# Kernel tuning notes

Hardware: AMD Instinct MI355X
Metric: run time of the kernel (lower is better)

Reference implementation:

```python
import jax, jax.numpy as jnp
import numpy as np

T, J, D = 65536, 512, 128

def setup_inputs() -> dict:
    key = jax.random.key(0)
    k1, k2 = jax.random.split(key)
    u = jax.random.normal(k1, (1, J, D), dtype=jnp.float32)
    s = jax.random.normal(k2, (T, J), dtype=jnp.float32)
    return {"u": u, "s": s}

def reference(u, s):
    # softmax over the query axis (axis=1 of s, matching tf softmax(s, axis=1))
    A = jax.nn.softmax(s, axis=1)          # [T, J]
    # sum_j A[t, j] * u[0, j, :]  == A @ u[0]
    c2q = jnp.einsum('tj,jd->td', A, u[0])  # [T, D]
    return c2q.T                            # [D, T], matching tf.transpose(c2q)
```

## Files before the change

kernel.cpp:

```cpp
#include <hip/hip_runtime.h>
#include <hip/hip_bf16.h>


constexpr int T_DIM = 65536;
constexpr int J_DIM = 512;
constexpr int D_DIM = 128;
constexpr int KK_STEPS = J_DIM / 32;
constexpr int NFRAG = 8;
constexpr int PF_DEPTH = 4;
constexpr int BP_ELEMS = KK_STEPS * NFRAG * 64;

typedef __attribute__((ext_vector_type(4))) float  f32x4;
typedef __attribute__((ext_vector_type(8))) short  s16x8;
typedef __attribute__((ext_vector_type(8))) __bf16 bf16x8;

__device__ __forceinline__ short f2bf_rne(float f) {
    unsigned u = __builtin_bit_cast(unsigned, f);
    u += 0x7fffu + ((u >> 16) & 1u);
    return (short)(u >> 16);
}

__global__ __launch_bounds__(256) void prep_b(const float* __restrict__ u,
                                              short* __restrict__ bp) {
    int tid = blockIdx.x * blockDim.x + threadIdx.x;
    if (tid >= BP_ELEMS) return;
    int l  = tid & 63;
    int nf = (tid >> 6) & (NFRAG - 1);
    int kk = tid >> 9;
    int d  = nf * 16 + (l & 15);
    int k0 = kk * 32 + 8 * (l >> 4);
    s16x8 o;
#pragma unroll
    for (int i = 0; i < 8; ++i)
        o[i] = f2bf_rne(u[(size_t)(k0 + i) * D_DIM + d]);
    *reinterpret_cast<s16x8*>(bp + (size_t)tid * 8) = o;
}

__global__ __launch_bounds__(512, 2) void c2q_main(const float* __restrict__ sm,
                                                   const short* __restrict__ bp,
                                                   float* __restrict__ out) {
    __shared__ s16x8 bsh[BP_ELEMS];

    const int tid  = threadIdx.x;
    const int l    = tid & 63;
    const int w    = tid >> 6;
    const int lmod = l & 15;
    const int lh   = l >> 4;
    const int r0   = blockIdx.x * 128 + w * 16;

    const float* sp = sm + (size_t)(r0 + lmod) * J_DIM + lh * 8;

    f32x4 sbuf[PF_DEPTH][2];
#pragma unroll
    for (int p = 0; p < PF_DEPTH; ++p) {
        sbuf[p][0] = *reinterpret_cast<const f32x4*>(sp + p * 32);
        sbuf[p][1] = *reinterpret_cast<const f32x4*>(sp + p * 32 + 4);
    }

    {
        const s16x8* bps = reinterpret_cast<const s16x8*>(bp);
#pragma unroll
        for (int it = 0; it < BP_ELEMS / 512; ++it)
            bsh[it * 512 + tid] = bps[it * 512 + tid];
    }
    __syncthreads();

    f32x4 acc[NFRAG];
#pragma unroll
    for (int nf = 0; nf < NFRAG; ++nf) acc[nf] = (f32x4){0.f, 0.f, 0.f, 0.f};
    float den = 0.f;

#pragma unroll
    for (int kk = 0; kk < KK_STEPS; ++kk) {
        f32x4 s0 = sbuf[kk & (PF_DEPTH - 1)][0];
        f32x4 s1 = sbuf[kk & (PF_DEPTH - 1)][1];
        if (kk + PF_DEPTH < KK_STEPS) {
            sbuf[kk & (PF_DEPTH - 1)][0] =
                *reinterpret_cast<const f32x4*>(sp + (kk + PF_DEPTH) * 32);
            sbuf[kk & (PF_DEPTH - 1)][1] =
                *reinterpret_cast<const f32x4*>(sp + (kk + PF_DEPTH) * 32 + 4);
        }
        float e0 = __expf(s0[0]), e1 = __expf(s0[1]);
        float e2 = __expf(s0[2]), e3 = __expf(s0[3]);
        float e4 = __expf(s1[0]), e5 = __expf(s1[1]);
        float e6 = __expf(s1[2]), e7 = __expf(s1[3]);
        den += ((e0 + e1) + (e2 + e3)) + ((e4 + e5) + (e6 + e7));
        s16x8 a;
        a[0] = f2bf_rne(e0); a[1] = f2bf_rne(e1);
        a[2] = f2bf_rne(e2); a[3] = f2bf_rne(e3);
        a[4] = f2bf_rne(e4); a[5] = f2bf_rne(e5);
        a[6] = f2bf_rne(e6); a[7] = f2bf_rne(e7);
        bf16x8 av = __builtin_bit_cast(bf16x8, a);
#pragma unroll
        for (int nf = 0; nf < NFRAG; ++nf) {
            bf16x8 bv = __builtin_bit_cast(bf16x8, bsh[(kk * NFRAG + nf) * 64 + l]);
            acc[nf] = __builtin_amdgcn_mfma_f32_16x16x32_bf16(av, bv, acc[nf], 0, 0, 0);
        }
        __builtin_amdgcn_sched_barrier(0);
    }

    den += __shfl_xor(den, 16, 64);
    den += __shfl_xor(den, 32, 64);
    float inv[4];
#pragma unroll
    for (int r = 0; r < 4; ++r)
        inv[r] = 1.0f / __shfl(den, 4 * lh + r, 64);

#pragma unroll
    for (int nf = 0; nf < NFRAG; ++nf) {
        f32x4 v;
#pragma unroll
        for (int r = 0; r < 4; ++r) v[r] = acc[nf][r] * inv[r];
        *reinterpret_cast<f32x4*>(out + (size_t)(nf * 16 + lmod) * T_DIM
                                  + r0 + 4 * lh) = v;
    }
}

extern "C" void kernel_launch(void* const* d_in, const int* in_sizes, int n_in,
                              void* d_out, int out_size, void* d_ws, size_t ws_size,
                              hipStream_t stream) {
    const float* u = (const float*)d_in[0];
    const float* s = (const float*)d_in[1];
    float* out = (float*)d_out;
    short* bp = (short*)d_ws;

    prep_b<<<(BP_ELEMS + 255) / 256, 256, 0, stream>>>(u, bp);
    c2q_main<<<T_DIM / 128, 512, 0, stream>>>(s, bp, out);
}
```

Baseline: 40.56 us.

## Process two row tiles per wave to reuse shared B fragments

```diff
diff --git a/kernel.cpp b/kernel.cpp
--- a/kernel.cpp
+++ b/kernel.cpp
@@ -46,15 +46,19 @@
     const int w    = tid >> 6;
     const int lmod = l & 15;
     const int lh   = l >> 4;
-    const int r0   = blockIdx.x * 128 + w * 16;
+    const int r0a  = blockIdx.x * 256 + w * 16;
+    const int r0b  = r0a + 128;
 
-    const float* sp = sm + (size_t)(r0 + lmod) * J_DIM + lh * 8;
+    const float* spA = sm + (size_t)(r0a + lmod) * J_DIM + lh * 8;
+    const float* spB = sm + (size_t)(r0b + lmod) * J_DIM + lh * 8;
 
-    f32x4 sbuf[PF_DEPTH][2];
+    f32x4 sbufA[PF_DEPTH][2], sbufB[PF_DEPTH][2];
 #pragma unroll
     for (int p = 0; p < PF_DEPTH; ++p) {
-        sbuf[p][0] = *reinterpret_cast<const f32x4*>(sp + p * 32);
-        sbuf[p][1] = *reinterpret_cast<const f32x4*>(sp + p * 32 + 4);
+        sbufA[p][0] = *reinterpret_cast<const f32x4*>(spA + p * 32);
+        sbufA[p][1] = *reinterpret_cast<const f32x4*>(spA + p * 32 + 4);
+        sbufB[p][0] = *reinterpret_cast<const f32x4*>(spB + p * 32);
+        sbufB[p][1] = *reinterpret_cast<const f32x4*>(spB + p * 32 + 4);
     }
 
     {
@@ -65,54 +69,83 @@
     }
     __syncthreads();
 
-    f32x4 acc[NFRAG];
+    f32x4 accA[NFRAG], accB[NFRAG];
 #pragma unroll
-    for (int nf = 0; nf < NFRAG; ++nf) acc[nf] = (f32x4){0.f, 0.f, 0.f, 0.f};
-    float den = 0.f;
+    for (int nf = 0; nf < NFRAG; ++nf) {
+        accA[nf] = (f32x4){0.f, 0.f, 0.f, 0.f};
+        accB[nf] = (f32x4){0.f, 0.f, 0.f, 0.f};
+    }
+    float denA = 0.f, denB = 0.f;
 
 #pragma unroll
     for (int kk = 0; kk < KK_STEPS; ++kk) {
-        f32x4 s0 = sbuf[kk & (PF_DEPTH - 1)][0];
-        f32x4 s1 = sbuf[kk & (PF_DEPTH - 1)][1];
+        f32x4 a0 = sbufA[kk & (PF_DEPTH - 1)][0];
+        f32x4 a1 = sbufA[kk & (PF_DEPTH - 1)][1];
+        f32x4 b0 = sbufB[kk & (PF_DEPTH - 1)][0];
+        f32x4 b1 = sbufB[kk & (PF_DEPTH - 1)][1];
         if (kk + PF_DEPTH < KK_STEPS) {
-            sbuf[kk & (PF_DEPTH - 1)][0] =
-                *reinterpret_cast<const f32x4*>(sp + (kk + PF_DEPTH) * 32);
-            sbuf[kk & (PF_DEPTH - 1)][1] =
-                *reinterpret_cast<const f32x4*>(sp + (kk + PF_DEPTH) * 32 + 4);
+            sbufA[kk & (PF_DEPTH - 1)][0] =
+                *reinterpret_cast<const f32x4*>(spA + (kk + PF_DEPTH) * 32);
+            sbufA[kk & (PF_DEPTH - 1)][1] =
+                *reinterpret_cast<const f32x4*>(spA + (kk + PF_DEPTH) * 32 + 4);
+            sbufB[kk & (PF_DEPTH - 1)][0] =
+                *reinterpret_cast<const f32x4*>(spB + (kk + PF_DEPTH) * 32);
+            sbufB[kk & (PF_DEPTH - 1)][1] =
+                *reinterpret_cast<const f32x4*>(spB + (kk + PF_DEPTH) * 32 + 4);
         }
-        float e0 = __expf(s0[0]), e1 = __expf(s0[1]);
-        float e2 = __expf(s0[2]), e3 = __expf(s0[3]);
-        float e4 = __expf(s1[0]), e5 = __expf(s1[1]);
-        float e6 = __expf(s1[2]), e7 = __expf(s1[3]);
-        den += ((e0 + e1) + (e2 + e3)) + ((e4 + e5) + (e6 + e7));
-        s16x8 a;
-        a[0] = f2bf_rne(e0); a[1] = f2bf_rne(e1);
-        a[2] = f2bf_rne(e2); a[3] = f2bf_rne(e3);
-        a[4] = f2bf_rne(e4); a[5] = f2bf_rne(e5);
-        a[6] = f2bf_rne(e6); a[7] = f2bf_rne(e7);
-        bf16x8 av = __builtin_bit_cast(bf16x8, a);
+        float ea0 = __expf(a0[0]), ea1 = __expf(a0[1]);
+        float ea2 = __expf(a0[2]), ea3 = __expf(a0[3]);
+        float ea4 = __expf(a1[0]), ea5 = __expf(a1[1]);
+        float ea6 = __expf(a1[2]), ea7 = __expf(a1[3]);
+        float eb0 = __expf(b0[0]), eb1 = __expf(b0[1]);
+        float eb2 = __expf(b0[2]), eb3 = __expf(b0[3]);
+        float eb4 = __expf(b1[0]), eb5 = __expf(b1[1]);
+        float eb6 = __expf(b1[2]), eb7 = __expf(b1[3]);
+        denA += ((ea0 + ea1) + (ea2 + ea3)) + ((ea4 + ea5) + (ea6 + ea7));
+        denB += ((eb0 + eb1) + (eb2 + eb3)) + ((eb4 + eb5) + (eb6 + eb7));
+        s16x8 pa, pb;
+        pa[0] = f2bf_rne(ea0); pa[1] = f2bf_rne(ea1);
+        pa[2] = f2bf_rne(ea2); pa[3] = f2bf_rne(ea3);
+        pa[4] = f2bf_rne(ea4); pa[5] = f2bf_rne(ea5);
+        pa[6] = f2bf_rne(ea6); pa[7] = f2bf_rne(ea7);
+        pb[0] = f2bf_rne(eb0); pb[1] = f2bf_rne(eb1);
+        pb[2] = f2bf_rne(eb2); pb[3] = f2bf_rne(eb3);
+        pb[4] = f2bf_rne(eb4); pb[5] = f2bf_rne(eb5);
+        pb[6] = f2bf_rne(eb6); pb[7] = f2bf_rne(eb7);
+        bf16x8 avA = __builtin_bit_cast(bf16x8, pa);
+        bf16x8 avB = __builtin_bit_cast(bf16x8, pb);
 #pragma unroll
         for (int nf = 0; nf < NFRAG; ++nf) {
             bf16x8 bv = __builtin_bit_cast(bf16x8, bsh[(kk * NFRAG + nf) * 64 + l]);
-            acc[nf] = __builtin_amdgcn_mfma_f32_16x16x32_bf16(av, bv, acc[nf], 0, 0, 0);
+            accA[nf] = __builtin_amdgcn_mfma_f32_16x16x32_bf16(avA, bv, accA[nf], 0, 0, 0);
+            accB[nf] = __builtin_amdgcn_mfma_f32_16x16x32_bf16(avB, bv, accB[nf], 0, 0, 0);
         }
         __builtin_amdgcn_sched_barrier(0);
     }
 
-    den += __shfl_xor(den, 16, 64);
-    den += __shfl_xor(den, 32, 64);
-    float inv[4];
+    denA += __shfl_xor(denA, 16, 64);
+    denA += __shfl_xor(denA, 32, 64);
+    denB += __shfl_xor(denB, 16, 64);
+    denB += __shfl_xor(denB, 32, 64);
+    float invA[4], invB[4];
 #pragma unroll
-    for (int r = 0; r < 4; ++r)
-        inv[r] = 1.0f / __shfl(den, 4 * lh + r, 64);
+    for (int r = 0; r < 4; ++r) {
+        invA[r] = 1.0f / __shfl(denA, 4 * lh + r, 64);
+        invB[r] = 1.0f / __shfl(denB, 4 * lh + r, 64);
+    }
 
 #pragma unroll
     for (int nf = 0; nf < NFRAG; ++nf) {
-        f32x4 v;
+        f32x4 va, vb;
 #pragma unroll
-        for (int r = 0; r < 4; ++r) v[r] = acc[nf][r] * inv[r];
+        for (int r = 0; r < 4; ++r) {
+            va[r] = accA[nf][r] * invA[r];
+            vb[r] = accB[nf][r] * invB[r];
+        }
         *reinterpret_cast<f32x4*>(out + (size_t)(nf * 16 + lmod) * T_DIM
-                                  + r0 + 4 * lh) = v;
+                                  + r0a + 4 * lh) = va;
+        *reinterpret_cast<f32x4*>(out + (size_t)(nf * 16 + lmod) * T_DIM
+                                  + r0b + 4 * lh) = vb;
     }
 }
 
@@ -125,5 +158,5 @@
     short* bp = (short*)d_ws;
 
     prep_b<<<(BP_ELEMS + 255) / 256, 256, 0, stream>>>(u, bp);
-    c2q_main<<<T_DIM / 128, 512, 0, stream>>>(s, bp, out);
+    c2q_main<<<T_DIM / 256, 512, 0, stream>>>(s, bp, out);
 }
```

After: 61.27 us. 1.51x slower.
